# Kernel tuning notes

Hardware: AMD Instinct MI355X
Metric: run time of the kernel (lower is better)

The kernel has to match this reference:

```python
import jax, jax.numpy as jnp
import numpy as np

NUM_LATENTS = 8192
LATENT_DIM = 256


def setup_inputs() -> dict:
    key = jax.random.key(0)
    kx, kw = jax.random.split(key)
    x = jax.random.normal(kx, (32, 512, LATENT_DIM), dtype=jnp.float32)
    # codebook init: uniform(-1/K, 1/K), matching nn.Embedding init in the module
    bound = 1.0 / NUM_LATENTS
    codebook = jax.random.uniform(
        kw, (NUM_LATENTS, LATENT_DIM), dtype=jnp.float32, minval=-bound, maxval=bound
    )
    return {"x": x, "codebook": codebook}


def reference(x, codebook):
    # torch.cdist(x, W) followed by argmin. Since sqrt is monotone, argmin over
    # squared Euclidean distance gives identical indices; we expand
    x2 = jnp.sum(x * x, axis=-1, keepdims=True)              # [B, T, 1]
    w2 = jnp.sum(codebook * codebook, axis=-1)               # [K]
    xw = jnp.einsum("btd,kd->btk", x, codebook)              # [B, T, K]
    dist2 = x2 - 2.0 * xw + w2                               # [B, T, K]
    indices = jnp.argmin(dist2, axis=-1)                     # [B, T] int
    z = codebook[indices]                                    # [B, T, D]
    # straight-through estimator: z_q = x + stop_grad(z - x)
    z_q = x + jax.lax.stop_gradient(z - x)
    return (z_q, z, x, indices)
```

## Files before the change

kernel.cpp:

```cpp
#include <hip/hip_runtime.h>
#include <hip/hip_bf16.h>
#include <cstddef>
#include <cstdint>

#define M_TOK   16384
#define N_CODE  8192
#define K_DIM   256
#define NSPLIT  4
#define BM      128
#define BN      128
#define BK      64

typedef short bf16x8 __attribute__((ext_vector_type(8)));
typedef float f32x4  __attribute__((ext_vector_type(4)));

__device__ __forceinline__ unsigned short f2bf_rne(float f) {
    unsigned u = __float_as_uint(f);
    unsigned r = u + 0x7FFFu + ((u >> 16) & 1u);
    return (unsigned short)(r >> 16);
}
__device__ __forceinline__ float bf2f(unsigned short h) {
    union { unsigned u; float f; } c; c.u = ((unsigned)h) << 16; return c.f;
}

__device__ __forceinline__ void gload16(const void* g, void* l) {
    __builtin_amdgcn_global_load_lds(
        (const __attribute__((address_space(1))) void*)g,
        (__attribute__((address_space(3))) void*)l, 16, 0, 0);
}

__global__ void vq_prep(const float* __restrict__ x, const float* __restrict__ cb,
                        unsigned short* __restrict__ xh, unsigned short* __restrict__ xl,
                        unsigned short* __restrict__ wh, unsigned short* __restrict__ wl,
                        float* __restrict__ x2, float* __restrict__ w2) {
    int gt   = blockIdx.x * blockDim.x + threadIdx.x;
    int row  = gt >> 6;
    int lane = gt & 63;
    if (row >= M_TOK + N_CODE) return;
    const float* src; unsigned short *dh, *dl; float* dn;
    if (row < M_TOK) {
        src = x + (size_t)row * K_DIM;
        dh = xh + (size_t)row * K_DIM; dl = xl + (size_t)row * K_DIM; dn = x2 + row;
    } else {
        int r = row - M_TOK;
        src = cb + (size_t)r * K_DIM;
        dh = wh + (size_t)r * K_DIM; dl = wl + (size_t)r * K_DIM; dn = w2 + r;
    }
    float4 v = ((const float4*)src)[lane];
    unsigned short h0 = f2bf_rne(v.x), h1 = f2bf_rne(v.y);
    unsigned short h2 = f2bf_rne(v.z), h3 = f2bf_rne(v.w);
    unsigned short l0 = f2bf_rne(v.x - bf2f(h0)), l1 = f2bf_rne(v.y - bf2f(h1));
    unsigned short l2 = f2bf_rne(v.z - bf2f(h2)), l3 = f2bf_rne(v.w - bf2f(h3));
    ushort4 hv; hv.x = h0; hv.y = h1; hv.z = h2; hv.w = h3;
    ushort4 lv; lv.x = l0; lv.y = l1; lv.z = l2; lv.w = l3;
    ((ushort4*)dh)[lane] = hv;
    ((ushort4*)dl)[lane] = lv;
    float s = v.x*v.x + v.y*v.y + v.z*v.z + v.w*v.w;
    #pragma unroll
    for (int off = 32; off > 0; off >>= 1) s += __shfl_down(s, off);
    if (lane == 0) *dn = s;
}

__global__ __launch_bounds__(256, 2)
void vq_main_mfma(const unsigned short* __restrict__ xh, const unsigned short* __restrict__ xl,
                  const unsigned short* __restrict__ wh, const unsigned short* __restrict__ wl,
                  const float* __restrict__ x2, const float* __restrict__ w2,
                  float* __restrict__ pminv, int* __restrict__ pmini) {
    __shared__ unsigned short xh_s[BM][BK];
    __shared__ unsigned short xl_s[BM][BK];
    __shared__ unsigned short wh_s[BN][BK];
    __shared__ unsigned short wl_s[BN][BK];
    __shared__ float red_d[BM][2];
    __shared__ int   red_i[BM][2];

    const int split = blockIdx.x;
    const int mtile = blockIdx.y;
    const int gm    = mtile * BM;
    const int tid   = threadIdx.x;
    const int w     = tid >> 6;
    const int lane  = tid & 63;
    const int wr    = w >> 1;
    const int wc    = w & 1;
    const int quad  = lane >> 4;
    const int l15   = lane & 15;

    const int w32   = w * 32;
    const int srl   = lane >> 3;
    const int sg    = (lane & 7) ^ srl;

    float x2r[16];
    #pragma unroll
    for (int rt = 0; rt < 4; ++rt)
        #pragma unroll
        for (int reg = 0; reg < 4; ++reg)
            x2r[rt*4+reg] = x2[gm + wr*64 + rt*16 + quad*4 + reg];

    float minv[16];
    int   mini[16];
    #pragma unroll
    for (int i = 0; i < 16; ++i) { minv[i] = 3.4e38f; mini[i] = 0; }

    const char* xhp = (const char*)xh;
    const char* xlp = (const char*)xl;
    const char* whp = (const char*)wh;
    const char* wlp = (const char*)wl;

    const int tiles = (N_CODE / NSPLIT) / BN;
    for (int tile = 0; tile < tiles; ++tile) {
        const int nb = split * (N_CODE / NSPLIT) + tile * BN;

        f32x4 acc[4][4];
        #pragma unroll
        for (int rt = 0; rt < 4; ++rt)
            #pragma unroll
            for (int ct = 0; ct < 4; ++ct)
                acc[rt][ct] = (f32x4){0.f, 0.f, 0.f, 0.f};

        for (int kc = 0; kc < K_DIM / BK; ++kc) {
            __syncthreads();
            #pragma unroll
            for (int i = 0; i < 4; ++i) {
                int rowl = w32 + i * 8 + srl;
                size_t xoff = (size_t)(gm + rowl) * (K_DIM*2) + kc*(BK*2) + sg*16;
                size_t woff = (size_t)(nb + rowl) * (K_DIM*2) + kc*(BK*2) + sg*16;
                unsigned ldso = (unsigned)w32 * (BK*2) + i * 1024;
                gload16(xhp + xoff, (char*)&xh_s[0][0] + ldso);
                gload16(xlp + xoff, (char*)&xl_s[0][0] + ldso);
                gload16(whp + woff, (char*)&wh_s[0][0] + ldso);
                gload16(wlp + woff, (char*)&wl_s[0][0] + ldso);
            }
            __syncthreads();

            #pragma unroll
            for (int ks = 0; ks < 2; ++ks) {
                bf16x8 ah[4], al[4], bh[4], bl[4];
                const int sl = ((ks << 2) + quad) ^ (l15 & 7);
                #pragma unroll
                for (int rt = 0; rt < 4; ++rt) {
                    int off = (wr*64 + rt*16 + l15) * (BK*2) + sl*16;
                    ah[rt] = *(const bf16x8*)((const char*)&xh_s[0][0] + off);
                    al[rt] = *(const bf16x8*)((const char*)&xl_s[0][0] + off);
                }
                #pragma unroll
                for (int ct = 0; ct < 4; ++ct) {
                    int off = (wc*64 + ct*16 + l15) * (BK*2) + sl*16;
                    bh[ct] = *(const bf16x8*)((const char*)&wh_s[0][0] + off);
                    bl[ct] = *(const bf16x8*)((const char*)&wl_s[0][0] + off);
                }
                #pragma unroll
                for (int rt = 0; rt < 4; ++rt)
                    #pragma unroll
                    for (int ct = 0; ct < 4; ++ct) {
                        acc[rt][ct] = __builtin_amdgcn_mfma_f32_16x16x32_bf16(al[rt], bh[ct], acc[rt][ct], 0, 0, 0);
                        acc[rt][ct] = __builtin_amdgcn_mfma_f32_16x16x32_bf16(ah[rt], bl[ct], acc[rt][ct], 0, 0, 0);
                        acc[rt][ct] = __builtin_amdgcn_mfma_f32_16x16x32_bf16(ah[rt], bh[ct], acc[rt][ct], 0, 0, 0);
                    }
            }
        }

        float w2c[4];
        int   cidx[4];
        #pragma unroll
        for (int ct = 0; ct < 4; ++ct) {
            cidx[ct] = nb + wc*64 + ct*16 + l15;
            w2c[ct]  = w2[cidx[ct]];
        }
        #pragma unroll
        for (int rt = 0; rt < 4; ++rt)
            #pragma unroll
            for (int ct = 0; ct < 4; ++ct) {
                #pragma unroll
                for (int reg = 0; reg < 4; ++reg) {
                    float d = (x2r[rt*4+reg] - 2.0f * acc[rt][ct][reg]) + w2c[ct];
                    int r16 = rt*4 + reg;
                    if (d < minv[r16]) { minv[r16] = d; mini[r16] = cidx[ct]; }
                }
            }
    }

    #pragma unroll
    for (int r16 = 0; r16 < 16; ++r16) {
        float d  = minv[r16];
        int   ix = mini[r16];
        #pragma unroll
        for (int off = 1; off < 16; off <<= 1) {
            float od = __shfl_xor(d, off);
            int   oi = __shfl_xor(ix, off);
            if (od < d || (od == d && oi < ix)) { d = od; ix = oi; }
        }
        if (l15 == 0) {
            int row_local = wr*64 + (r16 >> 2)*16 + quad*4 + (r16 & 3);
            red_d[row_local][wc] = d;
            red_i[row_local][wc] = ix;
        }
    }
    __syncthreads();
    if (tid < BM) {
        float d0 = red_d[tid][0], d1 = red_d[tid][1];
        int   i0 = red_i[tid][0], i1 = red_i[tid][1];
        float d; int ix;
        if (d1 < d0 || (d1 == d0 && i1 < i0)) { d = d1; ix = i1; } else { d = d0; ix = i0; }
        pminv[(size_t)(gm + tid) * NSPLIT + split] = d;
        pmini[(size_t)(gm + tid) * NSPLIT + split] = ix;
    }
}

__global__ void vq_gather(const float* __restrict__ x, const float* __restrict__ cb,
                          const float* __restrict__ pminv, const int* __restrict__ pmini,
                          float* __restrict__ out) {
    int t = blockIdx.x * blockDim.x + threadIdx.x;
    int m = t >> 6;
    int q = t & 63;

    float d  = pminv[(size_t)m * NSPLIT + (q & (NSPLIT-1))];
    int   ix = pmini[(size_t)m * NSPLIT + (q & (NSPLIT-1))];
    #pragma unroll
    for (int off = 1; off < NSPLIT; off <<= 1) {
        float od = __shfl_xor(d, off);
        int   oi = __shfl_xor(ix, off);
        if (od < d || (od == d && oi < ix)) { d = od; ix = oi; }
    }

    float4 xv = ((const float4*)x)[t];
    float4 zv = ((const float4*)cb)[(size_t)ix * 64 + q];
    float4 zq;
    zq.x = xv.x + (zv.x - xv.x);
    zq.y = xv.y + (zv.y - xv.y);
    zq.z = xv.z + (zv.z - xv.z);
    zq.w = xv.w + (zv.w - xv.w);
    float4* o = (float4*)out;
    const int ELEM4 = M_TOK * 64;
    o[t]           = zq;
    o[t + ELEM4]   = zv;
    o[t + 2*ELEM4] = xv;
    if (q == 0) out[(size_t)3 * M_TOK * K_DIM + m] = (float)ix;
}

extern "C" void kernel_launch(void* const* d_in, const int* in_sizes, int n_in,
                              void* d_out, int out_size, void* d_ws, size_t ws_size,
                              hipStream_t stream) {
    const float* x  = (const float*)d_in[0];
    const float* cb = (const float*)d_in[1];
    float* out = (float*)d_out;

    char* p = (char*)d_ws;
    unsigned short* xh = (unsigned short*)p;  p += (size_t)M_TOK  * K_DIM * 2;
    unsigned short* xl = (unsigned short*)p;  p += (size_t)M_TOK  * K_DIM * 2;
    unsigned short* wh = (unsigned short*)p;  p += (size_t)N_CODE * K_DIM * 2;
    unsigned short* wl = (unsigned short*)p;  p += (size_t)N_CODE * K_DIM * 2;
    float* x2    = (float*)p;  p += (size_t)M_TOK * 4;
    float* w2    = (float*)p;  p += (size_t)N_CODE * 4;
    float* pminv = (float*)p;  p += (size_t)M_TOK * NSPLIT * 4;
    int*   pmini = (int*)p;    p += (size_t)M_TOK * NSPLIT * 4;

    {
        int waves = M_TOK + N_CODE;
        vq_prep<<<(waves * 64 + 255) / 256, 256, 0, stream>>>(x, cb, xh, xl, wh, wl, x2, w2);
    }
    {
        dim3 grid(NSPLIT, M_TOK / BM);
        vq_main_mfma<<<grid, 256, 0, stream>>>(xh, xl, wh, wl, x2, w2, pminv, pmini);
    }
    {
        int t = M_TOK * (K_DIM / 4);
        vq_gather<<<t / 256, 256, 0, stream>>>(x, cb, pminv, pmini, out);
    }
}
```

Baseline: 281.8 us.

## Double-buffer LDS tiles with prefetch, remap blocks per XCD, raise MFMA priority

Halves the K chunk to 32 and double-buffers all four bf16 hi/lo operand tiles in LDS. The next step's global-to-LDS loads are issued before the MFMAs on the current buffer, so each step needs one barrier instead of two and memory latency can overlap compute. Block IDs are remapped so that blocks sharing an XCD reuse the same codebook split and token tiles in L2. MFMA sections are wrapped in s_setprio. The cost is twice as many loop iterations, more LDS per block and a dependence on the compiler placing vmcnt waits correctly before the barrier.

After: 292.3 us. 3.7% more time.

```diff
diff --git a/kernel.cpp b/kernel.cpp
--- a/kernel.cpp
+++ b/kernel.cpp
@@ -9,7 +9,10 @@
 #define NSPLIT  4
 #define BM      128
 #define BN      128
-#define BK      64
+#define BK      32
+#define KSTEPS  (K_DIM / BK)
+#define TILES   ((N_CODE / NSPLIT) / BN)
+#define TOTAL_STEPS (TILES * KSTEPS)
 
 typedef short bf16x8 __attribute__((ext_vector_type(8)));
 typedef float f32x4  __attribute__((ext_vector_type(4)));
@@ -66,16 +69,17 @@
                   const unsigned short* __restrict__ wh, const unsigned short* __restrict__ wl,
                   const float* __restrict__ x2, const float* __restrict__ w2,
                   float* __restrict__ pminv, int* __restrict__ pmini) {
-    __shared__ unsigned short xh_s[BM][BK];
-    __shared__ unsigned short xl_s[BM][BK];
-    __shared__ unsigned short wh_s[BN][BK];
-    __shared__ unsigned short wl_s[BN][BK];
+    __shared__ __align__(1024) unsigned short sbuf[2][4][BM][BK];
     __shared__ float red_d[BM][2];
     __shared__ int   red_i[BM][2];
 
-    const int split = blockIdx.x;
-    const int mtile = blockIdx.y;
+    const int fid   = blockIdx.y * NSPLIT + blockIdx.x;
+    const int xcd   = fid & 7;
+    const int jj    = fid >> 3;
+    const int split = xcd & 3;
+    const int mtile = ((xcd >> 2) << 6) + jj;
     const int gm    = mtile * BM;
+
     const int tid   = threadIdx.x;
     const int w     = tid >> 6;
     const int lane  = tid & 63;
@@ -85,8 +89,8 @@
     const int l15   = lane & 15;
 
     const int w32   = w * 32;
-    const int srl   = lane >> 3;
-    const int sg    = (lane & 7) ^ srl;
+    const int srow  = lane >> 2;
+    const int sg    = (lane & 3) ^ ((lane >> 3) & 3);
 
     float x2r[16];
     #pragma unroll
@@ -105,10 +109,38 @@
     const char* whp = (const char*)wh;
     const char* wlp = (const char*)wl;
 
-    const int tiles = (N_CODE / NSPLIT) / BN;
-    for (int tile = 0; tile < tiles; ++tile) {
-        const int nb = split * (N_CODE / NSPLIT) + tile * BN;
-
+    const size_t xr0 = (size_t)(gm + w32 + srow) * (K_DIM*2) + (size_t)sg*16;
+    const size_t xr1 = xr0 + (size_t)16 * (K_DIM*2);
+    const size_t wrb0 = (size_t)(w32 + srow) * (K_DIM*2) + (size_t)sg*16;
+    const size_t wrb1 = wrb0 + (size_t)16 * (K_DIM*2);
+    const unsigned ls0 = (unsigned)w32 * (BK*2);
+
+    #define STAGE(stepv)                                                            \
+    do {                                                                            \
+        const int   t_   = (stepv) >> 3;                                            \
+        const int   kcs_ = (stepv) & 7;                                             \
+        const int   b_   = (stepv) & 1;                                             \
+        const size_t ko_  = (size_t)kcs_ * (BK*2);                                  \
+        const size_t nbo_ = ((size_t)(split*(N_CODE/NSPLIT) + t_*BN)) * (K_DIM*2);  \
+        char* p0 = (char*)&sbuf[b_][0][0][0] + ls0;                                 \
+        char* p1 = (char*)&sbuf[b_][1][0][0] + ls0;                                 \
+        char* p2 = (char*)&sbuf[b_][2][0][0] + ls0;                                 \
+        char* p3 = (char*)&sbuf[b_][3][0][0] + ls0;                                 \
+        gload16(xhp + xr0 + ko_,        p0);                                        \
+        gload16(xhp + xr1 + ko_,        p0 + 1024);                                 \
+        gload16(xlp + xr0 + ko_,        p1);                                        \
+        gload16(xlp + xr1 + ko_,        p1 + 1024);                                 \
+        gload16(whp + nbo_ + wrb0 + ko_, p2);                                       \
+        gload16(whp + nbo_ + wrb1 + ko_, p2 + 1024);                                \
+        gload16(wlp + nbo_ + wrb0 + ko_, p3);                                       \
+        gload16(wlp + nbo_ + wrb1 + ko_, p3 + 1024);                                \
+    } while (0)
+
+    STAGE(0);
+
+    const int sl = quad ^ ((l15 >> 1) & 3);
+
+    for (int tile = 0; tile < TILES; ++tile) {
         f32x4 acc[4][4];
         #pragma unroll
         for (int rt = 0; rt < 4; ++rt)
@@ -116,48 +148,45 @@
             for (int ct = 0; ct < 4; ++ct)
                 acc[rt][ct] = (f32x4){0.f, 0.f, 0.f, 0.f};
 
-        for (int kc = 0; kc < K_DIM / BK; ++kc) {
+        #pragma unroll 2
+        for (int kcs = 0; kcs < KSTEPS; ++kcs) {
+            const int step = tile * KSTEPS + kcs;
             __syncthreads();
-            #pragma unroll
-            for (int i = 0; i < 4; ++i) {
-                int rowl = w32 + i * 8 + srl;
-                size_t xoff = (size_t)(gm + rowl) * (K_DIM*2) + kc*(BK*2) + sg*16;
-                size_t woff = (size_t)(nb + rowl) * (K_DIM*2) + kc*(BK*2) + sg*16;
-                unsigned ldso = (unsigned)w32 * (BK*2) + i * 1024;
-                gload16(xhp + xoff, (char*)&xh_s[0][0] + ldso);
-                gload16(xlp + xoff, (char*)&xl_s[0][0] + ldso);
-                gload16(whp + woff, (char*)&wh_s[0][0] + ldso);
-                gload16(wlp + woff, (char*)&wl_s[0][0] + ldso);
+            if (step + 1 < TOTAL_STEPS) STAGE(step + 1);
+
+            const int b = kcs & 1;
+            const char* xhb = (const char*)&sbuf[b][0][0][0];
+            const char* xlb = (const char*)&sbuf[b][1][0][0];
+            const char* whb = (const char*)&sbuf[b][2][0][0];
+            const char* wlb = (const char*)&sbuf[b][3][0][0];
+
+            bf16x8 ah[4], al[4], bh[4], bl[4];
+            #pragma unroll
+            for (int rt = 0; rt < 4; ++rt) {
+                const int off = (wr*64 + rt*16 + l15) * (BK*2) + sl*16;
+                ah[rt] = *(const bf16x8*)(xhb + off);
+                al[rt] = *(const bf16x8*)(xlb + off);
             }
-            __syncthreads();
-
-            #pragma unroll
-            for (int ks = 0; ks < 2; ++ks) {
-                bf16x8 ah[4], al[4], bh[4], bl[4];
-                const int sl = ((ks << 2) + quad) ^ (l15 & 7);
-                #pragma unroll
-                for (int rt = 0; rt < 4; ++rt) {
-                    int off = (wr*64 + rt*16 + l15) * (BK*2) + sl*16;
-                    ah[rt] = *(const bf16x8*)((const char*)&xh_s[0][0] + off);
-                    al[rt] = *(const bf16x8*)((const char*)&xl_s[0][0] + off);
-                }
+            #pragma unroll
+            for (int ct = 0; ct < 4; ++ct) {
+                const int off = (wc*64 + ct*16 + l15) * (BK*2) + sl*16;
+                bh[ct] = *(const bf16x8*)(whb + off);
+                bl[ct] = *(const bf16x8*)(wlb + off);
+            }
+
+            __builtin_amdgcn_s_setprio(1);
+            #pragma unroll
+            for (int rt = 0; rt < 4; ++rt)
                 #pragma unroll
                 for (int ct = 0; ct < 4; ++ct) {
-                    int off = (wc*64 + ct*16 + l15) * (BK*2) + sl*16;
-                    bh[ct] = *(const bf16x8*)((const char*)&wh_s[0][0] + off);
-                    bl[ct] = *(const bf16x8*)((const char*)&wl_s[0][0] + off);
+                    acc[rt][ct] = __builtin_amdgcn_mfma_f32_16x16x32_bf16(al[rt], bh[ct], acc[rt][ct], 0, 0, 0);
+                    acc[rt][ct] = __builtin_amdgcn_mfma_f32_16x16x32_bf16(ah[rt], bl[ct], acc[rt][ct], 0, 0, 0);
+                    acc[rt][ct] = __builtin_amdgcn_mfma_f32_16x16x32_bf16(ah[rt], bh[ct], acc[rt][ct], 0, 0, 0);
                 }
-                #pragma unroll
-                for (int rt = 0; rt < 4; ++rt)
-                    #pragma unroll
-                    for (int ct = 0; ct < 4; ++ct) {
-                        acc[rt][ct] = __builtin_amdgcn_mfma_f32_16x16x32_bf16(al[rt], bh[ct], acc[rt][ct], 0, 0, 0);
-                        acc[rt][ct] = __builtin_amdgcn_mfma_f32_16x16x32_bf16(ah[rt], bl[ct], acc[rt][ct], 0, 0, 0);
-                        acc[rt][ct] = __builtin_amdgcn_mfma_f32_16x16x32_bf16(ah[rt], bh[ct], acc[rt][ct], 0, 0, 0);
-                    }
-            }
-        }
-
+            __builtin_amdgcn_s_setprio(0);
+        }
+
+        const int nb = split * (N_CODE / NSPLIT) + tile * BN;
         float w2c[4];
         int   cidx[4];
         #pragma unroll
@@ -177,6 +206,7 @@
                 }
             }
     }
+    #undef STAGE
 
     #pragma unroll
     for (int r16 = 0; r16 < 16; ++r16) {
```

## Triple-buffer LDS loads with 512-thread blocks, BN=256 tiles and XCD-aware block mapping

Applied to the files above, without the earlier changes.

Restructures the main MFMA GEMM-argmin kernel into a 3-stage LDS ring: global-to-LDS loads for step+3 are issued right after the current fragments are read, with explicit vmcnt waits instead of two __syncthreads per k-chunk. Blocks grow to 512 threads (8 waves, 2x4 wave grid) covering BN=256 codes with BK=32, and the cross-wave reduction widens to four column groups. Block IDs are remapped so splits and M-tiles are spread across XCDs for L2 reuse, and s_setprio raises MFMA priority. The goal is to hide memory latency and cut barrier overhead. In exchange it adds hand-counted waitcnt logic that must match the loads issued per stage, and more LDS per block (about 144KB), which may limit occupancy.

Measured after the change: 295.7 us. 1.05x slower.

```diff
diff --git a/kernel.cpp b/kernel.cpp
--- a/kernel.cpp
+++ b/kernel.cpp
@@ -8,8 +8,16 @@
 #define K_DIM   256
 #define NSPLIT  4
 #define BM      128
-#define BN      128
-#define BK      64
+#define BN      256
+#define BK      32
+#define KSTEPS  (K_DIM / BK)
+#define TILES   ((N_CODE / NSPLIT) / BN)
+#define TOTAL_STEPS (TILES * KSTEPS)
+#define STEP_BYTES 49152
+#define XH_OFF 0
+#define XL_OFF 8192
+#define WH_OFF 16384
+#define WL_OFF 32768
 
 typedef short bf16x8 __attribute__((ext_vector_type(8)));
 typedef float f32x4  __attribute__((ext_vector_type(4)));
@@ -61,54 +69,74 @@
     if (lane == 0) *dn = s;
 }
 
-__global__ __launch_bounds__(256, 2)
+__global__ __launch_bounds__(512, 2)
 void vq_main_mfma(const unsigned short* __restrict__ xh, const unsigned short* __restrict__ xl,
                   const unsigned short* __restrict__ wh, const unsigned short* __restrict__ wl,
                   const float* __restrict__ x2, const float* __restrict__ w2,
                   float* __restrict__ pminv, int* __restrict__ pmini) {
-    __shared__ unsigned short xh_s[BM][BK];
-    __shared__ unsigned short xl_s[BM][BK];
-    __shared__ unsigned short wh_s[BN][BK];
-    __shared__ unsigned short wl_s[BN][BK];
-    __shared__ float red_d[BM][2];
-    __shared__ int   red_i[BM][2];
-
-    const int split = blockIdx.x;
-    const int mtile = blockIdx.y;
+    __shared__ __align__(1024) char sb[3][STEP_BYTES];
+    __shared__ float red_d[BM][4];
+    __shared__ int   red_i[BM][4];
+
+    const int fid   = blockIdx.y * NSPLIT + blockIdx.x;
+    const int xcd   = fid & 7;
+    const int split = xcd & 3;
+    const int mtile = ((xcd >> 2) << 6) + (fid >> 3);
     const int gm    = mtile * BM;
+
     const int tid   = threadIdx.x;
     const int w     = tid >> 6;
     const int lane  = tid & 63;
-    const int wr    = w >> 1;
-    const int wc    = w & 1;
+    const int wr    = w >> 2;
+    const int wc    = w & 3;
     const int quad  = lane >> 4;
     const int l15   = lane & 15;
 
-    const int w32   = w * 32;
-    const int srl   = lane >> 3;
-    const int sg    = (lane & 7) ^ srl;
-
-    float x2r[16];
-    #pragma unroll
-    for (int rt = 0; rt < 4; ++rt)
-        #pragma unroll
-        for (int reg = 0; reg < 4; ++reg)
-            x2r[rt*4+reg] = x2[gm + wr*64 + rt*16 + quad*4 + reg];
-
-    float minv[16];
-    int   mini[16];
-    #pragma unroll
-    for (int i = 0; i < 16; ++i) { minv[i] = 3.4e38f; mini[i] = 0; }
+    const int srow4 = lane >> 2;
+    const int sg    = (lane & 3) ^ ((lane >> 3) & 3);
 
     const char* xhp = (const char*)xh;
     const char* xlp = (const char*)xl;
     const char* whp = (const char*)wh;
     const char* wlp = (const char*)wl;
 
-    const int tiles = (N_CODE / NSPLIT) / BN;
-    for (int tile = 0; tile < tiles; ++tile) {
-        const int nb = split * (N_CODE / NSPLIT) + tile * BN;
-
+    const size_t xg0 = (size_t)(gm + w*16 + srow4) * (K_DIM*2) + (size_t)sg*16;
+    const size_t wg0 = (size_t)(w*32 + srow4) * (K_DIM*2) + (size_t)sg*16;
+    const size_t wg1 = wg0 + (size_t)16 * (K_DIM*2);
+    const unsigned lx = (unsigned)w*1024 + (unsigned)lane*16;
+    const unsigned lw = (unsigned)w*2048 + (unsigned)lane*16;
+
+    float x2r[16];
+    #pragma unroll
+    for (int rt = 0; rt < 4; ++rt)
+        #pragma unroll
+        for (int reg = 0; reg < 4; ++reg)
+            x2r[rt*4+reg] = x2[gm + wr*64 + rt*16 + quad*4 + reg];
+
+    float minv[16];
+    int   mini[16];
+    #pragma unroll
+    for (int i = 0; i < 16; ++i) { minv[i] = 3.4e38f; mini[i] = 0; }
+
+    auto stage = [&](int s, char* buf) {
+        const size_t kb  = (size_t)(s & (KSTEPS-1)) * (BK*2);
+        const size_t nbo = ((size_t)(split*(N_CODE/NSPLIT) + (s >> 3) * BN)) * (K_DIM*2);
+        gload16(xhp + xg0 + kb,        buf + XH_OFF + lx);
+        gload16(xlp + xg0 + kb,        buf + XL_OFF + lx);
+        gload16(whp + nbo + wg0 + kb,  buf + WH_OFF + lw);
+        gload16(whp + nbo + wg1 + kb,  buf + WH_OFF + lw + 1024);
+        gload16(wlp + nbo + wg0 + kb,  buf + WL_OFF + lw);
+        gload16(wlp + nbo + wg1 + kb,  buf + WL_OFF + lw + 1024);
+    };
+
+    char* bufA = &sb[0][0];
+    char* bufB = &sb[1][0];
+    char* bufC = &sb[2][0];
+    stage(0, bufA); stage(1, bufB); stage(2, bufC);
+
+    const int slb = (quad ^ ((l15 >> 1) & 3)) * 16;
+
+    for (int tile = 0; tile < TILES; ++tile) {
         f32x4 acc[4][4];
         #pragma unroll
         for (int rt = 0; rt < 4; ++rt)
@@ -116,48 +144,51 @@
             for (int ct = 0; ct < 4; ++ct)
                 acc[rt][ct] = (f32x4){0.f, 0.f, 0.f, 0.f};
 
-        for (int kc = 0; kc < K_DIM / BK; ++kc) {
-            __syncthreads();
-            #pragma unroll
-            for (int i = 0; i < 4; ++i) {
-                int rowl = w32 + i * 8 + srl;
-                size_t xoff = (size_t)(gm + rowl) * (K_DIM*2) + kc*(BK*2) + sg*16;
-                size_t woff = (size_t)(nb + rowl) * (K_DIM*2) + kc*(BK*2) + sg*16;
-                unsigned ldso = (unsigned)w32 * (BK*2) + i * 1024;
-                gload16(xhp + xoff, (char*)&xh_s[0][0] + ldso);
-                gload16(xlp + xoff, (char*)&xl_s[0][0] + ldso);
-                gload16(whp + woff, (char*)&wh_s[0][0] + ldso);
-                gload16(wlp + woff, (char*)&wl_s[0][0] + ldso);
+        for (int kcs = 0; kcs < KSTEPS; ++kcs) {
+            const int step = tile * KSTEPS + kcs;
+
+            if (step < TOTAL_STEPS - 2)       asm volatile("s_waitcnt vmcnt(12)" ::: "memory");
+            else if (step == TOTAL_STEPS - 2) asm volatile("s_waitcnt vmcnt(6)" ::: "memory");
+            else                              asm volatile("s_waitcnt vmcnt(0)" ::: "memory");
+            __builtin_amdgcn_s_barrier();
+            __builtin_amdgcn_sched_barrier(0);
+
+            bf16x8 ah[4], al[4], bh[4], bl[4];
+            #pragma unroll
+            for (int rt = 0; rt < 4; ++rt) {
+                const int off = (wr*64 + rt*16 + l15) * (BK*2) + slb;
+                ah[rt] = *(const bf16x8*)(bufA + XH_OFF + off);
+                al[rt] = *(const bf16x8*)(bufA + XL_OFF + off);
             }
-            __syncthreads();
-
-            #pragma unroll
-            for (int ks = 0; ks < 2; ++ks) {
-                bf16x8 ah[4], al[4], bh[4], bl[4];
-                const int sl = ((ks << 2) + quad) ^ (l15 & 7);
-                #pragma unroll
-                for (int rt = 0; rt < 4; ++rt) {
-                    int off = (wr*64 + rt*16 + l15) * (BK*2) + sl*16;
-                    ah[rt] = *(const bf16x8*)((const char*)&xh_s[0][0] + off);
-                    al[rt] = *(const bf16x8*)((const char*)&xl_s[0][0] + off);
-                }
+            #pragma unroll
+            for (int ct = 0; ct < 4; ++ct) {
+                const int off = (wc*64 + ct*16 + l15) * (BK*2) + slb;
+                bh[ct] = *(const bf16x8*)(bufA + WH_OFF + off);
+                bl[ct] = *(const bf16x8*)(bufA + WL_OFF + off);
+            }
+            asm volatile("s_waitcnt lgkmcnt(0)" ::: "memory");
+            __builtin_amdgcn_sched_barrier(0);
+            __builtin_amdgcn_s_barrier();
+            __builtin_amdgcn_sched_barrier(0);
+
+            const int sn = step + 3;
+            if (sn < TOTAL_STEPS) stage(sn, bufA);
+
+            __builtin_amdgcn_s_setprio(1);
+            #pragma unroll
+            for (int rt = 0; rt < 4; ++rt)
                 #pragma unroll
                 for (int ct = 0; ct < 4; ++ct) {
-                    int off = (wc*64 + ct*16 + l15) * (BK*2) + sl*16;
-                    bh[ct] = *(const bf16x8*)((const char*)&wh_s[0][0] + off);
-                    bl[ct] = *(const bf16x8*)((const char*)&wl_s[0][0] + off);
+                    acc[rt][ct] = __builtin_amdgcn_mfma_f32_16x16x32_bf16(al[rt], bh[ct], acc[rt][ct], 0, 0, 0);
+                    acc[rt][ct] = __builtin_amdgcn_mfma_f32_16x16x32_bf16(ah[rt], bl[ct], acc[rt][ct], 0, 0, 0);
+                    acc[rt][ct] = __builtin_amdgcn_mfma_f32_16x16x32_bf16(ah[rt], bh[ct], acc[rt][ct], 0, 0, 0);
                 }
-                #pragma unroll
-                for (int rt = 0; rt < 4; ++rt)
-                    #pragma unroll
-                    for (int ct = 0; ct < 4; ++ct) {
-                        acc[rt][ct] = __builtin_amdgcn_mfma_f32_16x16x32_bf16(al[rt], bh[ct], acc[rt][ct], 0, 0, 0);
-                        acc[rt][ct] = __builtin_amdgcn_mfma_f32_16x16x32_bf16(ah[rt], bl[ct], acc[rt][ct], 0, 0, 0);
-                        acc[rt][ct] = __builtin_amdgcn_mfma_f32_16x16x32_bf16(ah[rt], bh[ct], acc[rt][ct], 0, 0, 0);
-                    }
-            }
-        }
-
+            __builtin_amdgcn_s_setprio(0);
+
+            char* t = bufA; bufA = bufB; bufB = bufC; bufC = t;
+        }
+
+        const int nb = split * (N_CODE / NSPLIT) + tile * BN;
         float w2c[4];
         int   cidx[4];
         #pragma unroll
@@ -196,10 +227,14 @@
     }
     __syncthreads();
     if (tid < BM) {
-        float d0 = red_d[tid][0], d1 = red_d[tid][1];
-        int   i0 = red_i[tid][0], i1 = red_i[tid][1];
-        float d; int ix;
-        if (d1 < d0 || (d1 == d0 && i1 < i0)) { d = d1; ix = i1; } else { d = d0; ix = i0; }
+        float d  = red_d[tid][0];
+        int   ix = red_i[tid][0];
+        #pragma unroll
+        for (int j = 1; j < 4; ++j) {
+            float dj = red_d[tid][j];
+            int   ij = red_i[tid][j];
+            if (dj < d || (dj == d && ij < ix)) { d = dj; ix = ij; }
+        }
         pminv[(size_t)(gm + tid) * NSPLIT + split] = d;
         pmini[(size_t)(gm + tid) * NSPLIT + split] = ix;
     }
@@ -259,7 +294,7 @@
     }
     {
         dim3 grid(NSPLIT, M_TOK / BM);
-        vq_main_mfma<<<grid, 256, 0, stream>>>(xh, xl, wh, wl, x2, w2, pminv, pmini);
+        vq_main_mfma<<<grid, 512, 0, stream>>>(xh, xl, wh, wl, x2, w2, pminv, pmini);
     }
     {
         int t = M_TOK * (K_DIM / 4);
```

## Double-buffer x tiles in LDS and load codebook fragments directly from global

Applied to the files above, without the earlier changes.

The x hi/lo tiles are now double-buffered in LDS and the next k-step's x tile is prefetched while the current one is consumed, which removes one barrier per step. Codebook hi/lo fragments skip LDS and are read straight from global memory into registers. The block index is also remapped so that blocks sharing an XCD work on related splits and m-tiles, and x2 is reloaded per tile instead of being held in registers. This trades shared-memory staging of W for many uncached-pattern global loads, which may raise memory latency and cost cache bandwidth.

Measured after the change: 610.1 us. 116% more time.

```diff
diff --git a/kernel.cpp b/kernel.cpp
--- a/kernel.cpp
+++ b/kernel.cpp
@@ -10,6 +10,9 @@
 #define BM      128
 #define BN      128
 #define BK      64
+#define KSTEPS  (K_DIM / BK)
+#define TILES   ((N_CODE / NSPLIT) / BN)
+#define TOTAL_STEPS (TILES * KSTEPS)
 
 typedef short bf16x8 __attribute__((ext_vector_type(8)));
 typedef float f32x4  __attribute__((ext_vector_type(4)));
@@ -66,16 +69,17 @@
                   const unsigned short* __restrict__ wh, const unsigned short* __restrict__ wl,
                   const float* __restrict__ x2, const float* __restrict__ w2,
                   float* __restrict__ pminv, int* __restrict__ pmini) {
-    __shared__ unsigned short xh_s[BM][BK];
-    __shared__ unsigned short xl_s[BM][BK];
-    __shared__ unsigned short wh_s[BN][BK];
-    __shared__ unsigned short wl_s[BN][BK];
+    __shared__ unsigned short xh_s[2][BM][BK];
+    __shared__ unsigned short xl_s[2][BM][BK];
     __shared__ float red_d[BM][2];
     __shared__ int   red_i[BM][2];
 
-    const int split = blockIdx.x;
-    const int mtile = blockIdx.y;
+    const int fid   = blockIdx.y * NSPLIT + blockIdx.x;
+    const int xcd   = fid & 7;
+    const int split = xcd & 3;
+    const int mtile = ((xcd >> 2) << 6) + (fid >> 3);
     const int gm    = mtile * BM;
+
     const int tid   = threadIdx.x;
     const int w     = tid >> 6;
     const int lane  = tid & 63;
@@ -88,25 +92,33 @@
     const int srl   = lane >> 3;
     const int sg    = (lane & 7) ^ srl;
 
-    float x2r[16];
-    #pragma unroll
-    for (int rt = 0; rt < 4; ++rt)
-        #pragma unroll
-        for (int reg = 0; reg < 4; ++reg)
-            x2r[rt*4+reg] = x2[gm + wr*64 + rt*16 + quad*4 + reg];
-
-    float minv[16];
-    int   mini[16];
-    #pragma unroll
-    for (int i = 0; i < 16; ++i) { minv[i] = 3.4e38f; mini[i] = 0; }
-
     const char* xhp = (const char*)xh;
     const char* xlp = (const char*)xl;
     const char* whp = (const char*)wh;
     const char* wlp = (const char*)wl;
 
-    const int tiles = (N_CODE / NSPLIT) / BN;
-    for (int tile = 0; tile < tiles; ++tile) {
+    float minv[16];
+    int   mini[16];
+    #pragma unroll
+    for (int i = 0; i < 16; ++i) { minv[i] = 3.4e38f; mini[i] = 0; }
+
+    auto stage = [&](int step) {
+        const int kc = step & (KSTEPS - 1);
+        const int p  = step & 1;
+        #pragma unroll
+        for (int i = 0; i < 4; ++i) {
+            int rowl = w32 + i * 8 + srl;
+            size_t xoff = (size_t)(gm + rowl) * (K_DIM*2) + (size_t)kc*(BK*2) + (size_t)sg*16;
+            unsigned ldso = (unsigned)w32 * (BK*2) + i * 1024;
+            gload16(xhp + xoff, (char*)&xh_s[p][0][0] + ldso);
+            gload16(xlp + xoff, (char*)&xl_s[p][0][0] + ldso);
+        }
+    };
+
+    stage(0);
+    __syncthreads();
+
+    for (int tile = 0; tile < TILES; ++tile) {
         const int nb = split * (N_CODE / NSPLIT) + tile * BN;
 
         f32x4 acc[4][4];
@@ -116,48 +128,51 @@
             for (int ct = 0; ct < 4; ++ct)
                 acc[rt][ct] = (f32x4){0.f, 0.f, 0.f, 0.f};
 
-        for (int kc = 0; kc < K_DIM / BK; ++kc) {
-            __syncthreads();
-            #pragma unroll
-            for (int i = 0; i < 4; ++i) {
-                int rowl = w32 + i * 8 + srl;
-                size_t xoff = (size_t)(gm + rowl) * (K_DIM*2) + kc*(BK*2) + sg*16;
-                size_t woff = (size_t)(nb + rowl) * (K_DIM*2) + kc*(BK*2) + sg*16;
-                unsigned ldso = (unsigned)w32 * (BK*2) + i * 1024;
-                gload16(xhp + xoff, (char*)&xh_s[0][0] + ldso);
-                gload16(xlp + xoff, (char*)&xl_s[0][0] + ldso);
-                gload16(whp + woff, (char*)&wh_s[0][0] + ldso);
-                gload16(wlp + woff, (char*)&wl_s[0][0] + ldso);
-            }
-            __syncthreads();
+        #pragma unroll
+        for (int kc = 0; kc < KSTEPS; ++kc) {
+            const int step = tile * KSTEPS + kc;
+            const int p    = step & 1;
+
+            bf16x8 bh[2][4], bl[2][4];
+            #pragma unroll
+            for (int ks = 0; ks < 2; ++ks)
+                #pragma unroll
+                for (int ct = 0; ct < 4; ++ct) {
+                    size_t off = (size_t)(nb + wc*64 + ct*16 + l15) * (K_DIM*2)
+                               + (size_t)kc*(BK*2) + (size_t)(ks*4 + quad)*16;
+                    bh[ks][ct] = *(const bf16x8*)(whp + off);
+                    bl[ks][ct] = *(const bf16x8*)(wlp + off);
+                }
+
+            if (step + 1 < TOTAL_STEPS) stage(step + 1);
 
             #pragma unroll
             for (int ks = 0; ks < 2; ++ks) {
-                bf16x8 ah[4], al[4], bh[4], bl[4];
+                bf16x8 ah[4], al[4];
                 const int sl = ((ks << 2) + quad) ^ (l15 & 7);
                 #pragma unroll
                 for (int rt = 0; rt < 4; ++rt) {
                     int off = (wr*64 + rt*16 + l15) * (BK*2) + sl*16;
-                    ah[rt] = *(const bf16x8*)((const char*)&xh_s[0][0] + off);
-                    al[rt] = *(const bf16x8*)((const char*)&xl_s[0][0] + off);
-                }
-                #pragma unroll
-                for (int ct = 0; ct < 4; ++ct) {
-                    int off = (wc*64 + ct*16 + l15) * (BK*2) + sl*16;
-                    bh[ct] = *(const bf16x8*)((const char*)&wh_s[0][0] + off);
-                    bl[ct] = *(const bf16x8*)((const char*)&wl_s[0][0] + off);
+                    ah[rt] = *(const bf16x8*)((const char*)&xh_s[p][0][0] + off);
+                    al[rt] = *(const bf16x8*)((const char*)&xl_s[p][0][0] + off);
                 }
                 #pragma unroll
                 for (int rt = 0; rt < 4; ++rt)
                     #pragma unroll
                     for (int ct = 0; ct < 4; ++ct) {
-                        acc[rt][ct] = __builtin_amdgcn_mfma_f32_16x16x32_bf16(al[rt], bh[ct], acc[rt][ct], 0, 0, 0);
-                        acc[rt][ct] = __builtin_amdgcn_mfma_f32_16x16x32_bf16(ah[rt], bl[ct], acc[rt][ct], 0, 0, 0);
-                        acc[rt][ct] = __builtin_amdgcn_mfma_f32_16x16x32_bf16(ah[rt], bh[ct], acc[rt][ct], 0, 0, 0);
+                        acc[rt][ct] = __builtin_amdgcn_mfma_f32_16x16x32_bf16(al[rt], bh[ks][ct], acc[rt][ct], 0, 0, 0);
+                        acc[rt][ct] = __builtin_amdgcn_mfma_f32_16x16x32_bf16(ah[rt], bl[ks][ct], acc[rt][ct], 0, 0, 0);
+                        acc[rt][ct] = __builtin_amdgcn_mfma_f32_16x16x32_bf16(ah[rt], bh[ks][ct], acc[rt][ct], 0, 0, 0);
                     }
             }
-        }
-
+
+            __syncthreads();
+        }
+
+        f32x4 x2v[4];
+        #pragma unroll
+        for (int rt = 0; rt < 4; ++rt)
+            x2v[rt] = *(const f32x4*)(x2 + gm + wr*64 + rt*16 + quad*4);
         float w2c[4];
         int   cidx[4];
         #pragma unroll
@@ -171,7 +186,7 @@
             for (int ct = 0; ct < 4; ++ct) {
                 #pragma unroll
                 for (int reg = 0; reg < 4; ++reg) {
-                    float d = (x2r[rt*4+reg] - 2.0f * acc[rt][ct][reg]) + w2c[ct];
+                    float d = (x2v[rt][reg] - 2.0f * acc[rt][ct][reg]) + w2c[ct];
                     int r16 = rt*4 + reg;
                     if (d < minv[r16]) { minv[r16] = d; mini[r16] = cidx[ct]; }
                 }
```
